# Optimization experiments

Hardware: AMD Instinct MI355X
Metric: run time of the kernel (lower is better)

The kernel has to match this reference:

```python
import jax, jax.numpy as jnp
import numpy as np

N = 20000      # number of boxes / graph nodes
E = 160000     # random edges (before self-loops)
DIM = 1024     # feature dim (SIA default)


def setup_inputs() -> dict:
    key = jax.random.key(0)
    ks = jax.random.split(key, 12)
    feats = jax.random.normal(ks[0], (N, DIM), dtype=jnp.float32)
    boxes = jax.random.uniform(ks[1], (N, 4), dtype=jnp.float32)
    src = jax.random.randint(ks[2], (E,), 0, N, dtype=jnp.int32)
    dst = jax.random.randint(ks[3], (E,), 0, N, dtype=jnp.int32)
    loop = jnp.arange(N, dtype=jnp.int32)
    # dgl.add_self_loop: every node gets a self edge
    edges_src = jnp.concatenate([src, loop])
    edges_dst = jnp.concatenate([dst, loop])
    s = 0.02
    return {
        'feats': feats, 'boxes': boxes,
        'edges_src': edges_src, 'edges_dst': edges_dst,
        'w_pos1': jax.random.normal(ks[4], (4, DIM), jnp.float32) * s,
        'b_pos1': jnp.zeros((DIM,), jnp.float32),
        'w_pos2': jax.random.normal(ks[5], (DIM, DIM), jnp.float32) * s,
        'b_pos2': jnp.zeros((DIM,), jnp.float32),
        'w_g1': jax.random.normal(ks[6], (DIM, DIM), jnp.float32) * s,
        'b_g1': jnp.zeros((DIM,), jnp.float32),
        'w_g2': jax.random.normal(ks[7], (DIM, DIM), jnp.float32) * s,
        'b_g2': jnp.zeros((DIM,), jnp.float32),
    }


def _graph_conv(h, src, dst, w, b, n):
    # DGL GraphConv, norm='both', in_feats == out_feats => aggregate then matmul.
    ones = jnp.ones(src.shape, dtype=h.dtype)
    out_deg = jax.ops.segment_sum(ones, src, num_segments=n)
    in_deg = jax.ops.segment_sum(ones, dst, num_segments=n)
    norm_src = jnp.where(out_deg > 0, jax.lax.rsqrt(jnp.maximum(out_deg, 1.0)), 0.0)
    norm_dst = jnp.where(in_deg > 0, jax.lax.rsqrt(jnp.maximum(in_deg, 1.0)), 0.0)
    h = h * norm_src[:, None]
    agg = jax.ops.segment_sum(h[src], dst, num_segments=n)  # irregular gather/scatter
    agg = agg * norm_dst[:, None]
    return agg @ w + b


def reference(feats, boxes, edges_src, edges_dst,
              w_pos1, b_pos1, w_pos2, b_pos2,
              w_g1, b_g1, w_g2, b_g2):
    n = feats.shape[0]
    boxes = jnp.clip(boxes, -10.0, 10.0)
    pos = jax.nn.relu(boxes @ w_pos1 + b_pos1) @ w_pos2 + b_pos2
    h = feats + pos
    h = _graph_conv(h, edges_src, edges_dst, w_g1, b_g1, n)
    h = jax.nn.relu(h)  # dropout is identity in eval
    h = _graph_conv(h, edges_src, edges_dst, w_g2, b_g2, n)
    return h.mean(0)  # frame token [DIM]
```

## Files before the change

kernel.cpp:

```cpp
#include <hip/hip_runtime.h>
#include <hip/hip_bf16.h>
#include <stdint.h>

#define DIM 1024

typedef __attribute__((ext_vector_type(4))) float f32x4;
typedef __attribute__((ext_vector_type(8))) short short8;
typedef __attribute__((ext_vector_type(4))) short short4v;

__device__ __forceinline__ float bf2f(ushort u) {
    union { uint32_t u; float f; } c; c.u = ((uint32_t)u) << 16; return c.f;
}
__device__ __forceinline__ ushort f2bf(float f) {
    union { float f; uint32_t u; } c; c.f = f;
    uint32_t r = (c.u + 0x7fffu + ((c.u >> 16) & 1u)) >> 16;
    return (ushort)r;
}

__device__ __forceinline__ void async_copy16(void* lds, const void* g) {
    __builtin_amdgcn_global_load_lds((const __attribute__((address_space(1))) void*)g,
                                     (__attribute__((address_space(3))) void*)lds, 16, 0, 0);
}


__global__ void deg_kernel(const int* __restrict__ src, const int* __restrict__ dst,
                           int* out_deg, int* in_deg, int ee) {
    int e = blockIdx.x * 256 + threadIdx.x;
    if (e < ee) {
        atomicAdd(&out_deg[src[e]], 1);
        atomicAdd(&in_deg[dst[e]], 1);
    }
}

__global__ void norm_kernel(const int* __restrict__ out_deg, const int* __restrict__ in_deg,
                            float* ns, float* nd, int n) {
    int i = blockIdx.x * 256 + threadIdx.x;
    if (i < n) {
        int od = out_deg[i], id = in_deg[i];
        ns[i] = od > 0 ? rsqrtf((float)od) : 0.f;
        nd[i] = id > 0 ? rsqrtf((float)id) : 0.f;
    }
}

__global__ void csum_kernel(const int* __restrict__ src, const int* __restrict__ dst,
                            const float* __restrict__ nd, float* cw, int ee) {
    int e = blockIdx.x * 256 + threadIdx.x;
    if (e < ee) atomicAdd(&cw[src[e]], nd[dst[e]]);
}

__global__ void scan_kernel(const int* __restrict__ deg, int* row_ptr, int n) {
    __shared__ int wsum[16];
    __shared__ int carry_s;
    int tid = threadIdx.x, lane = tid & 63, wid = tid >> 6;
    if (tid == 0) carry_s = 0;
    __syncthreads();
    for (int base = 0; base < n; base += 1024) {
        int x = (base + tid < n) ? deg[base + tid] : 0;
        int v = x;
#pragma unroll
        for (int off = 1; off < 64; off <<= 1) {
            int u = __shfl_up(v, off);
            if (lane >= off) v += u;
        }
        if (lane == 63) wsum[wid] = v;
        __syncthreads();
        if (wid == 0 && lane < 16) {
            int wv = wsum[lane];
#pragma unroll
            for (int off = 1; off < 16; off <<= 1) {
                int wu = __shfl_up(wv, off);
                if (lane >= off) wv += wu;
            }
            wsum[lane] = wv;
        }
        __syncthreads();
        int waveoff = (wid > 0) ? wsum[wid - 1] : 0;
        if (base + tid < n) row_ptr[base + tid] = carry_s + waveoff + v - x;
        __syncthreads();
        if (tid == 0) carry_s += wsum[15];
        __syncthreads();
    }
}

__global__ void wnode_cursor_kernel(float* cw, const float* __restrict__ ns,
                                    const int* __restrict__ row_ptr, int* cursor, int n) {
    int i = blockIdx.x * 256 + threadIdx.x;
    if (i < n) {
        cw[i] *= ns[i];
        cursor[i] = row_ptr[i];
    }
}

__global__ void scatter_kernel(const int* __restrict__ src, const int* __restrict__ dst,
                               int* cursor, int* csr_src, int ee) {
    int e = blockIdx.x * 256 + threadIdx.x;
    if (e < ee) {
        int p = atomicAdd(&cursor[dst[e]], 1);
        csr_src[p] = src[e];
    }
}


__global__ __launch_bounds__(256) void posA_kernel(const float* __restrict__ boxes,
                                                   const float* __restrict__ w1,
                                                   const float* __restrict__ b1,
                                                   ushort* __restrict__ t, int n) {
    int row = blockIdx.x;
    if (row >= n) return;
    float b[4];
#pragma unroll
    for (int j = 0; j < 4; j++) {
        float v = boxes[row * 4 + j];
        b[j] = fminf(fmaxf(v, -10.f), 10.f);
    }
    int c0 = threadIdx.x * 4;
    short4v o;
#pragma unroll
    for (int q = 0; q < 4; q++) {
        int col = c0 + q;
        float v = b1[col];
#pragma unroll
        for (int j = 0; j < 4; j++) v = fmaf(b[j], w1[j * DIM + col], v);
        v = fmaxf(v, 0.f);
        o[q] = (short)f2bf(v);
    }
    *(short4v*)(t + (size_t)row * DIM + c0) = o;
}


__global__ __launch_bounds__(256) void transpose_bf16_kernel(const float* __restrict__ w,
                                                             ushort* __restrict__ wt) {
    __shared__ float tile[32][33];
    int bx = blockIdx.x, by = blockIdx.y;
    int tx = threadIdx.x & 31, ty = threadIdx.x >> 5;
#pragma unroll
    for (int r = 0; r < 32; r += 8)
        tile[ty + r][tx] = w[(size_t)(by * 32 + ty + r) * DIM + bx * 32 + tx];
    __syncthreads();
#pragma unroll
    for (int r = 0; r < 32; r += 8)
        wt[(size_t)(bx * 32 + ty + r) * DIM + by * 32 + tx] = f2bf(tile[tx][ty + r]);
}


template <int EPI>
__global__ __launch_bounds__(256) void gemm_kernel(
    const ushort* __restrict__ A, const ushort* __restrict__ Bt,
    const float* __restrict__ bias, const float* __restrict__ feats,
    const float* __restrict__ nsrc, ushort* __restrict__ outp,
    int mtiles, int mreal) {
    __shared__ __align__(128) ushort ldsA[2][128 * 64];
    __shared__ __align__(128) ushort ldsB[2][128 * 64];
    int j = blockIdx.x;
    int xcd = j & 7, k = j >> 3;
    int bm = xcd + 8 * (k >> 3);
    int bn = k & 7;
    if (bm >= mtiles) return;

    int tid = threadIdx.x, lane = tid & 63, wid = tid >> 6;
    int wm = wid >> 1, wn = wid & 1;

    f32x4 acc[4][4];
#pragma unroll
    for (int m = 0; m < 4; m++)
#pragma unroll
        for (int n = 0; n < 4; n++) acc[m][n] = (f32x4){0.f, 0.f, 0.f, 0.f};

    int srow = wid * 8 + (lane >> 3);
    int sseg = (lane & 7) ^ (lane >> 3);
    const ushort* gA = A + (size_t)(bm * 128 + srow) * DIM + sseg * 8;
    const ushort* gB = Bt + (size_t)(bn * 128 + srow) * DIM + sseg * 8;

    int r16 = lane & 15, khi = lane >> 4, rx = lane & 7;

    auto stage = [&](int buf, int kt) {
        ushort* lA = &ldsA[buf][(wid * 8) * 64];
        ushort* lB = &ldsB[buf][(wid * 8) * 64];
#pragma unroll
        for (int c = 0; c < 4; c++) {
            async_copy16(lA + c * 2048, gA + (size_t)c * 32 * DIM + kt * 64);
            async_copy16(lB + c * 2048, gB + (size_t)c * 32 * DIM + kt * 64);
        }
    };

    stage(0, 0);
    asm volatile("s_waitcnt vmcnt(0)" ::: "memory");
    __syncthreads();
    int cur = 0;
    for (int kt = 0; kt < DIM / 64; ++kt) {
        if (kt < DIM / 64 - 1) stage(cur ^ 1, kt + 1);
#pragma unroll
        for (int kk = 0; kk < 2; kk++) {
            short8 af[4], bfv[4];
#pragma unroll
            for (int m = 0; m < 4; m++) {
                int row = wm * 64 + m * 16 + r16;
                int seg = (kk * 4 + khi) ^ rx;
                af[m] = *(const short8*)&ldsA[cur][row * 64 + seg * 8];
            }
#pragma unroll
            for (int n = 0; n < 4; n++) {
                int row = wn * 64 + n * 16 + r16;
                int seg = (kk * 4 + khi) ^ rx;
                bfv[n] = *(const short8*)&ldsB[cur][row * 64 + seg * 8];
            }
#pragma unroll
            for (int m = 0; m < 4; m++)
#pragma unroll
                for (int n = 0; n < 4; n++)
                    acc[m][n] = __builtin_amdgcn_mfma_f32_16x16x32_bf16(af[m], bfv[n], acc[m][n], 0, 0, 0);
        }
        if (kt < DIM / 64 - 1) {
            asm volatile("s_waitcnt vmcnt(0)" ::: "memory");
            __syncthreads();
            cur ^= 1;
        }
    }

    int colbase = bn * 128 + wn * 64;
    int rowbase = bm * 128 + wm * 64 + khi * 4;
    if (EPI == 1) {
#pragma unroll
        for (int m = 0; m < 4; m++) {
#pragma unroll
            for (int jj = 0; jj < 4; jj++) {
                int r = rowbase + m * 16 + jj;
                if (r < mreal) {
                    float ns = nsrc[r];
#pragma unroll
                    for (int n = 0; n < 4; n++) {
                        int col = colbase + n * 16 + r16;
                        float v = acc[m][n][jj] + bias[col] + feats[(size_t)r * DIM + col];
                        outp[(size_t)r * DIM + col] = f2bf(v * ns);
                    }
                }
            }
        }
    } else {
#pragma unroll
        for (int m = 0; m < 4; m++) {
#pragma unroll
            for (int jj = 0; jj < 4; jj++) {
                int r = rowbase + m * 16 + jj;
                if (r < mreal) {
#pragma unroll
                    for (int n = 0; n < 4; n++) {
                        int col = colbase + n * 16 + r16;
                        outp[(size_t)r * DIM + col] = f2bf(acc[m][n][jj]);
                    }
                }
            }
        }
    }
}


__global__ __launch_bounds__(256) void agg2_kernel(
    const ushort* __restrict__ z, const int* __restrict__ row_ptr,
    const int* __restrict__ in_deg, const int* __restrict__ csr_src,
    const float* __restrict__ ndst, const float* __restrict__ wnode,
    const float* __restrict__ bg1, float* __restrict__ vec, int n) {
    __shared__ float red[DIM];
    int lane = threadIdx.x & 63, wid = threadIdx.x >> 6;
    int wave = blockIdx.x * 4 + wid;
    int nwaves = gridDim.x * 4;
    int c0 = lane * 8;

    float bv[16];
#pragma unroll
    for (int t = 0; t < 8; t++) { bv[t] = bg1[c0 + t]; bv[8 + t] = bg1[512 + c0 + t]; }
    float part[16];
#pragma unroll
    for (int t = 0; t < 16; t++) part[t] = 0.f;

    for (int node = wave; node < n; node += nwaves) {
        int start = row_ptr[node], cnt = in_deg[node];
        float a[16];
#pragma unroll
        for (int t = 0; t < 16; t++) a[t] = 0.f;
        int e = 0;
        for (; e + 2 <= cnt; e += 2) {
            const ushort* r0 = z + (size_t)csr_src[start + e] * DIM;
            const ushort* r1 = z + (size_t)csr_src[start + e + 1] * DIM;
            short8 v00 = *(const short8*)(r0 + c0);
            short8 v01 = *(const short8*)(r0 + 512 + c0);
            short8 v10 = *(const short8*)(r1 + c0);
            short8 v11 = *(const short8*)(r1 + 512 + c0);
#pragma unroll
            for (int t = 0; t < 8; t++) {
                a[t]     += bf2f((ushort)v00[t]) + bf2f((ushort)v10[t]);
                a[8 + t] += bf2f((ushort)v01[t]) + bf2f((ushort)v11[t]);
            }
        }
        if (e < cnt) {
            const ushort* r0 = z + (size_t)csr_src[start + e] * DIM;
            short8 v00 = *(const short8*)(r0 + c0);
            short8 v01 = *(const short8*)(r0 + 512 + c0);
#pragma unroll
            for (int t = 0; t < 8; t++) {
                a[t]     += bf2f((ushort)v00[t]);
                a[8 + t] += bf2f((ushort)v01[t]);
            }
        }
        float nd = ndst[node], w = wnode[node];
#pragma unroll
        for (int t = 0; t < 16; t++)
            part[t] = fmaf(w, fmaxf(fmaf(nd, a[t], bv[t]), 0.f), part[t]);
    }

    if (wid == 0) {
#pragma unroll
        for (int t = 0; t < 8; t++) { red[c0 + t] = part[t]; red[512 + c0 + t] = part[8 + t]; }
    }
    __syncthreads();
    for (int w = 1; w < 4; ++w) {
        if (wid == w) {
#pragma unroll
            for (int t = 0; t < 8; t++) { red[c0 + t] += part[t]; red[512 + c0 + t] += part[8 + t]; }
        }
        __syncthreads();
    }
    for (int c = threadIdx.x; c < DIM; c += 256) atomicAdd(&vec[c], red[c]);
}


__global__ __launch_bounds__(256) void final_kernel(const float* __restrict__ vec,
                                                    const float* __restrict__ w2,
                                                    const float* __restrict__ b2,
                                                    float* out, float invn) {
    int d = blockIdx.x * 256 + threadIdx.x;
    int kb = blockIdx.y * 128;
    float acc = 0.f;
#pragma unroll 4
    for (int k = 0; k < 128; k++) acc = fmaf(vec[kb + k], w2[(size_t)(kb + k) * DIM + d], acc);
    float add = acc * invn + (blockIdx.y == 0 ? b2[d] : 0.f);
    atomicAdd(&out[d], add);
}


extern "C" void kernel_launch(void* const* d_in, const int* in_sizes, int n_in,
                              void* d_out, int out_size, void* d_ws, size_t ws_size,
                              hipStream_t stream) {
    const float* feats  = (const float*)d_in[0];
    const float* boxes  = (const float*)d_in[1];
    const int*   esrc   = (const int*)d_in[2];
    const int*   edst   = (const int*)d_in[3];
    const float* w_pos1 = (const float*)d_in[4];
    const float* b_pos1 = (const float*)d_in[5];
    const float* w_pos2 = (const float*)d_in[6];
    const float* b_pos2 = (const float*)d_in[7];
    const float* w_g1   = (const float*)d_in[8];
    const float* b_g1   = (const float*)d_in[9];
    const float* w_g2   = (const float*)d_in[10];
    const float* b_g2   = (const float*)d_in[11];

    int n = in_sizes[0] / DIM;
    int ee = in_sizes[2];
    int mtiles = (n + 127) / 128;
    int groups = (mtiles + 7) / 8;
    int gemm_grid = groups * 64;

    char* p = (char*)d_ws;
    auto alloc = [&](size_t bytes) -> char* {
        char* r = p;
        p += (bytes + 255) & ~((size_t)255);
        return r;
    };
    size_t mp = (size_t)mtiles * 128;
    ushort* t_z    = (ushort*)alloc(mp * DIM * 2);
    ushort* hs     = (ushort*)alloc(mp * DIM * 2);
    ushort* wt1    = (ushort*)alloc((size_t)DIM * DIM * 2);
    ushort* wt2    = (ushort*)alloc((size_t)DIM * DIM * 2);
    char* zero_base = p;
    int*   out_deg = (int*)alloc((size_t)n * 4);
    int*   in_deg  = (int*)alloc((size_t)n * 4);
    float* cw      = (float*)alloc((size_t)n * 4);
    float* vec     = (float*)alloc((size_t)DIM * 4);
    size_t zero_bytes = (size_t)(p - zero_base);
    float* nsrc    = (float*)alloc((size_t)n * 4);
    float* ndst    = (float*)alloc((size_t)n * 4);
    int*   row_ptr = (int*)alloc((size_t)(n + 1) * 4);
    int*   cursor  = (int*)alloc((size_t)n * 4);
    int*   csr_src = (int*)alloc((size_t)ee * 4);

    hipMemsetAsync(zero_base, 0, zero_bytes, stream);
    hipMemsetAsync(d_out, 0, (size_t)out_size * 4, stream);

    int eb = (ee + 255) / 256;
    int nb = (n + 255) / 256;

    deg_kernel<<<eb, 256, 0, stream>>>(esrc, edst, out_deg, in_deg, ee);
    posA_kernel<<<n, 256, 0, stream>>>(boxes, w_pos1, b_pos1, t_z, n);
    transpose_bf16_kernel<<<dim3(32, 32), 256, 0, stream>>>(w_pos2, wt1);
    transpose_bf16_kernel<<<dim3(32, 32), 256, 0, stream>>>(w_g1, wt2);
    norm_kernel<<<nb, 256, 0, stream>>>(out_deg, in_deg, nsrc, ndst, n);
    csum_kernel<<<eb, 256, 0, stream>>>(esrc, edst, ndst, cw, ee);
    scan_kernel<<<1, 1024, 0, stream>>>(in_deg, row_ptr, n);
    wnode_cursor_kernel<<<nb, 256, 0, stream>>>(cw, nsrc, row_ptr, cursor, n);
    scatter_kernel<<<eb, 256, 0, stream>>>(esrc, edst, cursor, csr_src, ee);

    gemm_kernel<1><<<gemm_grid, 256, 0, stream>>>(t_z, wt1, b_pos2, feats, nsrc, hs, mtiles, n);
    gemm_kernel<0><<<gemm_grid, 256, 0, stream>>>(hs, wt2, nullptr, nullptr, nullptr, t_z, mtiles, n);
    agg2_kernel<<<1024, 256, 0, stream>>>(t_z, row_ptr, in_deg, csr_src, ndst, cw, b_g1, vec, n);
    final_kernel<<<dim3(4, 8), 256, 0, stream>>>(vec, w_g2, b_g2, (float*)d_out, 1.0f / (float)n);
}
```

Measured before the change: 449.2 us.

## Use 8-wave GEMM blocks with single-barrier pipeline, widen posA and agg unroll

The GEMM now launches 512 threads (8 waves) per 128x128 tile, so each wave owns a 32x64 sub-tile. Its double-buffered loop waits on partial vmcnt with raw s_barrier instead of a full drain and __syncthreads. posA becomes a grid-stride, one-wave-per-row kernel with 16-wide stores, the aggregation loop is unrolled to four edges, and the cursor copy is folded into the scan kernel to drop one pass. Together these aim to hide more latency and cut launch and per-iteration overhead, at the cost of fewer accumulators per wave and tighter barrier ordering.

Result: faster. 425.0 us (-5.4%).

```diff
diff --git a/kernel.cpp b/kernel.cpp
--- a/kernel.cpp
+++ b/kernel.cpp
@@ -6,7 +6,6 @@
 
 typedef __attribute__((ext_vector_type(4))) float f32x4;
 typedef __attribute__((ext_vector_type(8))) short short8;
-typedef __attribute__((ext_vector_type(4))) short short4v;
 
 __device__ __forceinline__ float bf2f(ushort u) {
     union { uint32_t u; float f; } c; c.u = ((uint32_t)u) << 16; return c.f;
@@ -48,7 +47,7 @@
     if (e < ee) atomicAdd(&cw[src[e]], nd[dst[e]]);
 }
 
-__global__ void scan_kernel(const int* __restrict__ deg, int* row_ptr, int n) {
+__global__ void scan_kernel(const int* __restrict__ deg, int* row_ptr, int* cursor, int n) {
     __shared__ int wsum[16];
     __shared__ int carry_s;
     int tid = threadIdx.x, lane = tid & 63, wid = tid >> 6;
@@ -75,20 +74,20 @@
         }
         __syncthreads();
         int waveoff = (wid > 0) ? wsum[wid - 1] : 0;
-        if (base + tid < n) row_ptr[base + tid] = carry_s + waveoff + v - x;
+        if (base + tid < n) {
+            int ex = carry_s + waveoff + v - x;
+            row_ptr[base + tid] = ex;
+            cursor[base + tid] = ex;
+        }
         __syncthreads();
         if (tid == 0) carry_s += wsum[15];
         __syncthreads();
     }
 }
 
-__global__ void wnode_cursor_kernel(float* cw, const float* __restrict__ ns,
-                                    const int* __restrict__ row_ptr, int* cursor, int n) {
+__global__ void wnode_kernel(float* cw, const float* __restrict__ ns, int n) {
     int i = blockIdx.x * 256 + threadIdx.x;
-    if (i < n) {
-        cw[i] *= ns[i];
-        cursor[i] = row_ptr[i];
-    }
+    if (i < n) cw[i] *= ns[i];
 }
 
 __global__ void scatter_kernel(const int* __restrict__ src, const int* __restrict__ dst,
@@ -105,26 +104,31 @@
                                                    const float* __restrict__ w1,
                                                    const float* __restrict__ b1,
                                                    ushort* __restrict__ t, int n) {
-    int row = blockIdx.x;
-    if (row >= n) return;
-    float b[4];
-#pragma unroll
-    for (int j = 0; j < 4; j++) {
-        float v = boxes[row * 4 + j];
-        b[j] = fminf(fmaxf(v, -10.f), 10.f);
-    }
-    int c0 = threadIdx.x * 4;
-    short4v o;
-#pragma unroll
-    for (int q = 0; q < 4; q++) {
-        int col = c0 + q;
-        float v = b1[col];
-#pragma unroll
-        for (int j = 0; j < 4; j++) v = fmaf(b[j], w1[j * DIM + col], v);
-        v = fmaxf(v, 0.f);
-        o[q] = (short)f2bf(v);
-    }
-    *(short4v*)(t + (size_t)row * DIM + c0) = o;
+    int lane = threadIdx.x & 63, wid = threadIdx.x >> 6;
+    int wave = blockIdx.x * 4 + wid, nw = gridDim.x * 4;
+    int c0 = lane * 16;
+    for (int row = wave; row < n; row += nw) {
+        float b[4];
+#pragma unroll
+        for (int j = 0; j < 4; j++) {
+            float v = boxes[row * 4 + j];
+            b[j] = fminf(fmaxf(v, -10.f), 10.f);
+        }
+        short8 o[2];
+#pragma unroll
+        for (int h = 0; h < 2; h++) {
+#pragma unroll
+            for (int q = 0; q < 8; q++) {
+                int col = c0 + h * 8 + q;
+                float v = b1[col];
+#pragma unroll
+                for (int j = 0; j < 4; j++) v = fmaf(b[j], w1[j * DIM + col], v);
+                o[h][q] = (short)f2bf(fmaxf(v, 0.f));
+            }
+        }
+        *(short8*)(t + (size_t)row * DIM + c0) = o[0];
+        *(short8*)(t + (size_t)row * DIM + c0 + 8) = o[1];
+    }
 }
 
 
@@ -144,7 +148,7 @@
 
 
 template <int EPI>
-__global__ __launch_bounds__(256) void gemm_kernel(
+__global__ __launch_bounds__(512, 4) void gemm_kernel(
     const ushort* __restrict__ A, const ushort* __restrict__ Bt,
     const float* __restrict__ bias, const float* __restrict__ feats,
     const float* __restrict__ nsrc, ushort* __restrict__ outp,
@@ -152,85 +156,87 @@
     __shared__ __align__(128) ushort ldsA[2][128 * 64];
     __shared__ __align__(128) ushort ldsB[2][128 * 64];
     int j = blockIdx.x;
-    int xcd = j & 7, k = j >> 3;
-    int bm = xcd + 8 * (k >> 3);
-    int bn = k & 7;
+    int xcd = j & 7, kq = j >> 3;
+    int bm = xcd + 8 * (kq >> 3);
+    int bn = kq & 7;
     if (bm >= mtiles) return;
 
     int tid = threadIdx.x, lane = tid & 63, wid = tid >> 6;
     int wm = wid >> 1, wn = wid & 1;
 
-    f32x4 acc[4][4];
-#pragma unroll
-    for (int m = 0; m < 4; m++)
-#pragma unroll
-        for (int n = 0; n < 4; n++) acc[m][n] = (f32x4){0.f, 0.f, 0.f, 0.f};
+    f32x4 acc[2][4];
+#pragma unroll
+    for (int m = 0; m < 2; m++)
+#pragma unroll
+        for (int nn = 0; nn < 4; nn++) acc[m][nn] = (f32x4){0.f, 0.f, 0.f, 0.f};
 
     int srow = wid * 8 + (lane >> 3);
     int sseg = (lane & 7) ^ (lane >> 3);
     const ushort* gA = A + (size_t)(bm * 128 + srow) * DIM + sseg * 8;
     const ushort* gB = Bt + (size_t)(bn * 128 + srow) * DIM + sseg * 8;
-
-    int r16 = lane & 15, khi = lane >> 4, rx = lane & 7;
+    int ldsoff0 = (wid * 8) * 64;
+
+    int r16 = lane & 15, khi = lane >> 4;
 
     auto stage = [&](int buf, int kt) {
-        ushort* lA = &ldsA[buf][(wid * 8) * 64];
-        ushort* lB = &ldsB[buf][(wid * 8) * 64];
-#pragma unroll
-        for (int c = 0; c < 4; c++) {
-            async_copy16(lA + c * 2048, gA + (size_t)c * 32 * DIM + kt * 64);
-            async_copy16(lB + c * 2048, gB + (size_t)c * 32 * DIM + kt * 64);
+#pragma unroll
+        for (int c = 0; c < 2; c++) {
+            async_copy16(&ldsA[buf][ldsoff0 + c * 64 * 64], gA + (size_t)c * 64 * DIM + kt * 64);
+            async_copy16(&ldsB[buf][ldsoff0 + c * 64 * 64], gB + (size_t)c * 64 * DIM + kt * 64);
         }
     };
 
     stage(0, 0);
-    asm volatile("s_waitcnt vmcnt(0)" ::: "memory");
-    __syncthreads();
     int cur = 0;
     for (int kt = 0; kt < DIM / 64; ++kt) {
-        if (kt < DIM / 64 - 1) stage(cur ^ 1, kt + 1);
+        if (kt + 1 < DIM / 64) {
+            stage(cur ^ 1, kt + 1);
+            asm volatile("s_waitcnt vmcnt(4)" ::: "memory");
+        } else {
+            asm volatile("s_waitcnt vmcnt(0)" ::: "memory");
+        }
+        __builtin_amdgcn_s_barrier();
+        __builtin_amdgcn_sched_barrier(0);
 #pragma unroll
         for (int kk = 0; kk < 2; kk++) {
-            short8 af[4], bfv[4];
-#pragma unroll
-            for (int m = 0; m < 4; m++) {
-                int row = wm * 64 + m * 16 + r16;
-                int seg = (kk * 4 + khi) ^ rx;
+            short8 af[2], bfv[4];
+#pragma unroll
+            for (int m = 0; m < 2; m++) {
+                int row = wm * 32 + m * 16 + r16;
+                int seg = (kk * 4 + khi) ^ (row & 7);
                 af[m] = *(const short8*)&ldsA[cur][row * 64 + seg * 8];
             }
 #pragma unroll
-            for (int n = 0; n < 4; n++) {
-                int row = wn * 64 + n * 16 + r16;
-                int seg = (kk * 4 + khi) ^ rx;
-                bfv[n] = *(const short8*)&ldsB[cur][row * 64 + seg * 8];
-            }
-#pragma unroll
-            for (int m = 0; m < 4; m++)
-#pragma unroll
-                for (int n = 0; n < 4; n++)
-                    acc[m][n] = __builtin_amdgcn_mfma_f32_16x16x32_bf16(af[m], bfv[n], acc[m][n], 0, 0, 0);
-        }
-        if (kt < DIM / 64 - 1) {
-            asm volatile("s_waitcnt vmcnt(0)" ::: "memory");
-            __syncthreads();
-            cur ^= 1;
-        }
+            for (int nn = 0; nn < 4; nn++) {
+                int row = wn * 64 + nn * 16 + r16;
+                int seg = (kk * 4 + khi) ^ (row & 7);
+                bfv[nn] = *(const short8*)&ldsB[cur][row * 64 + seg * 8];
+            }
+#pragma unroll
+            for (int m = 0; m < 2; m++)
+#pragma unroll
+                for (int nn = 0; nn < 4; nn++)
+                    acc[m][nn] = __builtin_amdgcn_mfma_f32_16x16x32_bf16(af[m], bfv[nn], acc[m][nn], 0, 0, 0);
+        }
+        __builtin_amdgcn_sched_barrier(0);
+        __builtin_amdgcn_s_barrier();
+        cur ^= 1;
     }
 
     int colbase = bn * 128 + wn * 64;
-    int rowbase = bm * 128 + wm * 64 + khi * 4;
+    int rowbase = bm * 128 + wm * 32 + khi * 4;
     if (EPI == 1) {
 #pragma unroll
-        for (int m = 0; m < 4; m++) {
+        for (int m = 0; m < 2; m++) {
 #pragma unroll
             for (int jj = 0; jj < 4; jj++) {
                 int r = rowbase + m * 16 + jj;
                 if (r < mreal) {
                     float ns = nsrc[r];
 #pragma unroll
-                    for (int n = 0; n < 4; n++) {
-                        int col = colbase + n * 16 + r16;
-                        float v = acc[m][n][jj] + bias[col] + feats[(size_t)r * DIM + col];
+                    for (int nn = 0; nn < 4; nn++) {
+                        int col = colbase + nn * 16 + r16;
+                        float v = acc[m][nn][jj] + bias[col] + feats[(size_t)r * DIM + col];
                         outp[(size_t)r * DIM + col] = f2bf(v * ns);
                     }
                 }
@@ -238,15 +244,15 @@
         }
     } else {
 #pragma unroll
-        for (int m = 0; m < 4; m++) {
+        for (int m = 0; m < 2; m++) {
 #pragma unroll
             for (int jj = 0; jj < 4; jj++) {
                 int r = rowbase + m * 16 + jj;
                 if (r < mreal) {
 #pragma unroll
-                    for (int n = 0; n < 4; n++) {
-                        int col = colbase + n * 16 + r16;
-                        outp[(size_t)r * DIM + col] = f2bf(acc[m][n][jj]);
+                    for (int nn = 0; nn < 4; nn++) {
+                        int col = colbase + nn * 16 + r16;
+                        outp[(size_t)r * DIM + col] = f2bf(acc[m][nn][jj]);
                     }
                 }
             }
@@ -279,20 +285,28 @@
 #pragma unroll
         for (int t = 0; t < 16; t++) a[t] = 0.f;
         int e = 0;
-        for (; e + 2 <= cnt; e += 2) {
+        for (; e + 4 <= cnt; e += 4) {
             const ushort* r0 = z + (size_t)csr_src[start + e] * DIM;
             const ushort* r1 = z + (size_t)csr_src[start + e + 1] * DIM;
+            const ushort* r2 = z + (size_t)csr_src[start + e + 2] * DIM;
+            const ushort* r3 = z + (size_t)csr_src[start + e + 3] * DIM;
             short8 v00 = *(const short8*)(r0 + c0);
             short8 v01 = *(const short8*)(r0 + 512 + c0);
             short8 v10 = *(const short8*)(r1 + c0);
             short8 v11 = *(const short8*)(r1 + 512 + c0);
+            short8 v20 = *(const short8*)(r2 + c0);
+            short8 v21 = *(const short8*)(r2 + 512 + c0);
+            short8 v30 = *(const short8*)(r3 + c0);
+            short8 v31 = *(const short8*)(r3 + 512 + c0);
 #pragma unroll
             for (int t = 0; t < 8; t++) {
-                a[t]     += bf2f((ushort)v00[t]) + bf2f((ushort)v10[t]);
-                a[8 + t] += bf2f((ushort)v01[t]) + bf2f((ushort)v11[t]);
-            }
-        }
-        if (e < cnt) {
+                a[t]     += (bf2f((ushort)v00[t]) + bf2f((ushort)v10[t])) +
+                            (bf2f((ushort)v20[t]) + bf2f((ushort)v30[t]));
+                a[8 + t] += (bf2f((ushort)v01[t]) + bf2f((ushort)v11[t])) +
+                            (bf2f((ushort)v21[t]) + bf2f((ushort)v31[t]));
+            }
+        }
+        for (; e < cnt; e++) {
             const ushort* r0 = z + (size_t)csr_src[start + e] * DIM;
             short8 v00 = *(const short8*)(r0 + c0);
             short8 v01 = *(const short8*)(r0 + 512 + c0);
@@ -390,17 +404,17 @@
     int nb = (n + 255) / 256;
 
     deg_kernel<<<eb, 256, 0, stream>>>(esrc, edst, out_deg, in_deg, ee);
-    posA_kernel<<<n, 256, 0, stream>>>(boxes, w_pos1, b_pos1, t_z, n);
+    posA_kernel<<<256, 256, 0, stream>>>(boxes, w_pos1, b_pos1, t_z, n);
     transpose_bf16_kernel<<<dim3(32, 32), 256, 0, stream>>>(w_pos2, wt1);
     transpose_bf16_kernel<<<dim3(32, 32), 256, 0, stream>>>(w_g1, wt2);
     norm_kernel<<<nb, 256, 0, stream>>>(out_deg, in_deg, nsrc, ndst, n);
     csum_kernel<<<eb, 256, 0, stream>>>(esrc, edst, ndst, cw, ee);
-    scan_kernel<<<1, 1024, 0, stream>>>(in_deg, row_ptr, n);
-    wnode_cursor_kernel<<<nb, 256, 0, stream>>>(cw, nsrc, row_ptr, cursor, n);
+    scan_kernel<<<1, 1024, 0, stream>>>(in_deg, row_ptr, cursor, n);
+    wnode_kernel<<<nb, 256, 0, stream>>>(cw, nsrc, n);
     scatter_kernel<<<eb, 256, 0, stream>>>(esrc, edst, cursor, csr_src, ee);
 
-    gemm_kernel<1><<<gemm_grid, 256, 0, stream>>>(t_z, wt1, b_pos2, feats, nsrc, hs, mtiles, n);
-    gemm_kernel<0><<<gemm_grid, 256, 0, stream>>>(hs, wt2, nullptr, nullptr, nullptr, t_z, mtiles, n);
+    gemm_kernel<1><<<gemm_grid, 512, 0, stream>>>(t_z, wt1, b_pos2, feats, nsrc, hs, mtiles, n);
+    gemm_kernel<0><<<gemm_grid, 512, 0, stream>>>(hs, wt2, nullptr, nullptr, nullptr, t_z, mtiles, n);
     agg2_kernel<<<1024, 256, 0, stream>>>(t_z, row_ptr, in_deg, csr_src, ndst, cw, b_g1, vec, n);
     final_kernel<<<dim3(4, 8), 256, 0, stream>>>(vec, w_g2, b_g2, (float*)d_out, 1.0f / (float)n);
 }
```
